# Performance work log

Measured on AMD Instinct MI355X. Metric: run time of the kernel, lower is better.

Reference implementation:

```python
import jax, jax.numpy as jnp
import numpy as np

B, S, H, D = 256, 512, 256, 512  # batch, n_seq, n_hid, n_dim
LN_EPS = 1e-5


def _xavier(key, fan_out, fan_in):
    lim = (6.0 / (fan_in + fan_out)) ** 0.5
    return jax.random.uniform(key, (fan_out, fan_in), jnp.float32, -lim, lim)


def setup_inputs() -> dict:
    key = jax.random.key(0)
    ks = jax.random.split(key, 10)
    x = jax.random.normal(ks[0], (B, S, D), jnp.float32)
    k_w = _xavier(ks[1], H, D)
    q_w = _xavier(ks[2], H, D)
    v_w = _xavier(ks[3], H, D)
    lb = 1.0 / (D ** 0.5)
    k_b = jax.random.uniform(ks[4], (H,), jnp.float32, -lb, lb)
    q_b = jax.random.uniform(ks[5], (H,), jnp.float32, -lb, lb)
    v_b = jax.random.uniform(ks[6], (H,), jnp.float32, -lb, lb)
    attn_bias = jax.random.normal(ks[7], (S, H), jnp.float32)
    ln_g = jnp.ones((H,), jnp.float32)
    ln_b = jnp.zeros((H,), jnp.float32)
    lo = 1.0 / ((S * H) ** 0.5)
    out_w = jax.random.uniform(ks[8], (D, S * H), jnp.float32, -lo, lo)
    out_b = jax.random.uniform(ks[9], (D,), jnp.float32, -lo, lo)
    return {"x": x, "k_w": k_w, "k_b": k_b, "q_w": q_w, "q_b": q_b,
            "v_w": v_w, "v_b": v_b, "attn_bias": attn_bias,
            "ln_g": ln_g, "ln_b": ln_b, "out_w": out_w, "out_b": out_b}


def reference(x, k_w, k_b, q_w, q_b, v_w, v_b, attn_bias, ln_g, ln_b, out_w, out_b):
    # projections: [B,S,D] -> [B,S,H]
    k = jnp.einsum('bsd,hd->bsh', x, k_w) + k_b
    q = jnp.einsum('bsd,hd->bsh', x, q_w) + q_b
    v = jnp.einsum('bsd,hd->bsh', x, v_w) + v_b
    # scores = k^T q, scaled by BATCH size^-0.5 (faithful to v.shape[0]**-0.5)
    scale = x.shape[0] ** (-0.5)
    scores = jnp.einsum('bsh,bsg->bhg', k, q) * scale  # [B,H,H]
    weight = jax.nn.softmax(scores, axis=1)
    out = jnp.einsum('bsh,bhg->bsg', v, weight)  # [B,S,H]
    out = out + attn_bias
    # LayerNorm over last dim
    mu = out.mean(-1, keepdims=True)
    var = out.var(-1, keepdims=True)
    out = (out - mu) * jax.lax.rsqrt(var + LN_EPS) * ln_g + ln_b
    # dropout is identity in eval mode; exact (erf) GELU matches torch default
    out = jax.nn.gelu(out, approximate=False)
    out = out.reshape(out.shape[0], S * H)
    out = out @ out_w.T + out_b  # [B,D]
    return out[:, None, :]  # [B,1,D]
```

## Files before the change

### kernel.cpp

```cpp
#include <hip/hip_runtime.h>
#include <hip/hip_bf16.h>
#include <math.h>

#define B_ 256
#define S_ 512
#define H_ 256
#define D_ 512

typedef __bf16 bf16;
typedef __bf16 bf16x8 __attribute__((ext_vector_type(8)));
typedef float  f32x4  __attribute__((ext_vector_type(4)));
typedef unsigned short u16x8 __attribute__((ext_vector_type(8)));
typedef unsigned short u16x4 __attribute__((ext_vector_type(4)));

#define MFMA(a, b, c) __builtin_amdgcn_mfma_f32_16x16x32_bf16((a), (b), (c), 0, 0, 0)

__device__ __forceinline__ int swz(int row, int kbyte) {
  return (row * 128 + kbyte) ^ ((row & 7) << 4);
}
__device__ __forceinline__ unsigned short bfbits(float f) {
  bf16 h = (bf16)f;
  union { bf16 b; unsigned short u; } c; c.b = h; return c.u;
}
__device__ __forceinline__ bf16x8 cvt8(const float* __restrict__ p) {
  f32x4 a = *(const f32x4*)p;
  f32x4 b = *(const f32x4*)(p + 4);
  bf16x8 r;
  r[0] = (bf16)a[0]; r[1] = (bf16)a[1]; r[2] = (bf16)a[2]; r[3] = (bf16)a[3];
  r[4] = (bf16)b[0]; r[5] = (bf16)b[1]; r[6] = (bf16)b[2]; r[7] = (bf16)b[3];
  return r;
}
__device__ __forceinline__ void gload16(const unsigned short* g, unsigned char* l) {
  __builtin_amdgcn_global_load_lds(
      (const __attribute__((address_space(1))) unsigned int*)g,
      (__attribute__((address_space(3))) unsigned int*)l, 16, 0, 0);
}

__global__ __launch_bounds__(256) void k_convw(
    const float* __restrict__ kw, const float* __restrict__ qw,
    const float* __restrict__ vw, unsigned short* __restrict__ wc)
{
  const int r = blockIdx.x;
  const float* src = (r < 256) ? kw + (size_t)r * 512
                   : (r < 512) ? qw + (size_t)(r - 256) * 512
                               : vw + (size_t)(r - 512) * 512;
  const int c = threadIdx.x * 2;
  wc[(size_t)r * 512 + c]     = bfbits(src[c]);
  wc[(size_t)r * 512 + c + 1] = bfbits(src[c + 1]);
}

__global__ __launch_bounds__(256) void k_proj3(
    const float* __restrict__ x,
    const unsigned short* __restrict__ wc,
    const float* __restrict__ kbi, const float* __restrict__ qbi,
    const float* __restrict__ vbi,
    unsigned short* __restrict__ k_t, unsigned short* __restrict__ q_t,
    unsigned short* __restrict__ v_o, int nwg)
{
  __shared__ __align__(16) unsigned char sA[16384];
  __shared__ __align__(16) unsigned char sB[32768];

  const int o = blockIdx.x;
  const int cpx = nwg >> 3;
  const int a = (o & 7) * cpx + (o >> 3);
  const int mt = a / 6;
  const int nb = a - mt * 6;
  const int m0 = mt * 128;
  const int n0 = nb * 128;
  const int region = nb >> 1;
  const int h0 = (nb & 1) * 128;
  const float* __restrict__ Bi = (region == 0) ? kbi : (region == 1) ? qbi : vbi;

  const int tid = threadIdx.x;
  const int lane = tid & 63;
  const int wid = tid >> 6;
  const int wm = wid >> 1;
  const int wn = wid & 1;
  const int l15 = lane & 15;
  const int lr = lane >> 3;
  const int lk = (lane & 7) << 3;

  f32x4 acc[4][4];
#pragma unroll
  for (int i = 0; i < 4; ++i)
#pragma unroll
    for (int j = 0; j < 4; ++j) acc[i][j] = (f32x4){0.f, 0.f, 0.f, 0.f};

  auto issueB = [&](int kt, int buf) {
#pragma unroll
    for (int i = 0; i < 4; ++i) {
      const int chunk = wid * 4 + i;
      const int row = chunk * 8 + lr;
      gload16(wc + (size_t)(n0 + row) * 512 + kt * 64 + lk,
              sB + buf * 16384 + chunk * 1024);
    }
  };

  f32x4 pa[4], pb[4];
  auto loadA = [&](int kt) {
#pragma unroll
    for (int i = 0; i < 4; ++i) {
      int c = tid + i * 256;
      int row = c >> 3, kc = (c & 7) * 8;
      const float* p = x + (size_t)(m0 + row) * D_ + kt * 64 + kc;
      pa[i] = *(const f32x4*)p;
      pb[i] = *(const f32x4*)(p + 4);
    }
  };

  loadA(0);
  issueB(0, 0);

  for (int kt = 0; kt < 8; ++kt) {
    const int cur = kt & 1;
    __builtin_amdgcn_s_barrier();
    __builtin_amdgcn_sched_barrier(0);
#pragma unroll
    for (int i = 0; i < 4; ++i) {
      int c = tid + i * 256;
      int row = c >> 3, kc = (c & 7) * 8;
      bf16x8 r;
      r[0] = (bf16)pa[i][0]; r[1] = (bf16)pa[i][1];
      r[2] = (bf16)pa[i][2]; r[3] = (bf16)pa[i][3];
      r[4] = (bf16)pb[i][0]; r[5] = (bf16)pb[i][1];
      r[6] = (bf16)pb[i][2]; r[7] = (bf16)pb[i][3];
      *(bf16x8*)(sA + swz(row, kc * 2)) = r;
    }
    if (kt < 7) issueB(kt + 1, cur ^ 1);
    if (kt < 7) asm volatile("s_waitcnt vmcnt(4) lgkmcnt(0)" ::: "memory");
    else        asm volatile("s_waitcnt vmcnt(0) lgkmcnt(0)" ::: "memory");
    __builtin_amdgcn_s_barrier();
    __builtin_amdgcn_sched_barrier(0);
    if (kt < 7) loadA(kt + 1);
#pragma unroll
    for (int ks = 0; ks < 2; ++ks) {
      const int kb2 = ks * 64 + ((lane >> 4) << 4);
      bf16x8 av[4], bv[4];
#pragma unroll
      for (int f = 0; f < 4; ++f)
        av[f] = *(const bf16x8*)(sA + swz(wm * 64 + f * 16 + l15, kb2));
#pragma unroll
      for (int f = 0; f < 4; ++f)
        bv[f] = *(const bf16x8*)(sB + cur * 16384 + (wn * 64 + f * 16 + l15) * 128 + kb2);
#pragma unroll
      for (int fm = 0; fm < 4; ++fm)
#pragma unroll
        for (int fn = 0; fn < 4; ++fn)
          acc[fm][fn] = MFMA(av[fm], bv[fn], acc[fm][fn]);
    }
    __builtin_amdgcn_sched_barrier(0);
  }

  const int b = m0 >> 9;
  const int sbase = m0 & 511;
  const int r4 = (lane >> 4) * 4;
#pragma unroll
  for (int fn = 0; fn < 4; ++fn) {
    const int hcol = h0 + wn * 64 + fn * 16 + l15;
    const float bias = Bi[hcol];
#pragma unroll
    for (int fm = 0; fm < 4; ++fm) {
      const int s = sbase + wm * 64 + fm * 16 + r4;
      if (region < 2) {
        unsigned short* dst = ((region == 0) ? k_t : q_t) +
                              (size_t)b * (H_ * S_) + (size_t)hcol * S_ + s;
        u16x4 ov;
#pragma unroll
        for (int j = 0; j < 4; ++j) ov[j] = bfbits(acc[fm][fn][j] + bias);
        *(u16x4*)dst = ov;
      } else {
#pragma unroll
        for (int j = 0; j < 4; ++j)
          v_o[(size_t)b * (S_ * H_) + (size_t)(s + j) * H_ + hcol] =
              bfbits(acc[fm][fn][j] + bias);
      }
    }
  }
}

__global__ __launch_bounds__(1024, 4) void k_attn(
    const unsigned short* __restrict__ k_t,
    const unsigned short* __restrict__ q_t,
    const unsigned short* __restrict__ v_o,
    const float* __restrict__ attn_bias,
    const float* __restrict__ lng, const float* __restrict__ lnb,
    unsigned short* __restrict__ act)
{
  __shared__ __align__(16) unsigned char sm[163840];
  unsigned char* sP = sm;
  float* redm = (float*)(sm + 131072);
  float* reds = (float*)(sm + 131072 + 4096);
  float* lbuf = (float*)(sm + 147456);

  const int tid = threadIdx.x;
  const int lane = tid & 63;
  const int wid = tid >> 6;
  const int l15 = lane & 15;
  const int l16 = lane >> 4;
  const int b = blockIdx.x;
  const int wh = wid >> 2;
  const int wq = wid & 3;

  const unsigned short* __restrict__ Kb = k_t + (size_t)b * (H_ * S_);
  const unsigned short* __restrict__ Qb = q_t + (size_t)b * (H_ * S_);
  const unsigned short* __restrict__ Vb = v_o + (size_t)b * (S_ * H_);

  const int srow8 = lane >> 3;
  const int scol16 = (lane & 7) ^ srow8;

  auto stage1 = [&](int t, int buf) {
#pragma unroll
    for (int i = 0; i < 2; ++i) {
      const int cb = wid * 2 + i;
      const int row = cb * 8 + srow8;
      gload16(Kb + (size_t)row * S_ + t * 64 + scol16 * 8,
              sm + buf * 65536 + cb * 1024);
      gload16(Qb + (size_t)row * S_ + t * 64 + scol16 * 8,
              sm + buf * 65536 + 32768 + cb * 1024);
    }
  };

  f32x4 acc1[4][4];
#pragma unroll
  for (int i = 0; i < 4; ++i)
#pragma unroll
    for (int j = 0; j < 4; ++j) acc1[i][j] = (f32x4){0.f, 0.f, 0.f, 0.f};

  stage1(0, 0);
  for (int t = 0; t < 8; ++t) {
    const int cur = t & 1;
    if (t < 7) stage1(t + 1, cur ^ 1);
    if (t < 7) asm volatile("s_waitcnt vmcnt(4)" ::: "memory");
    else       asm volatile("s_waitcnt vmcnt(0)" ::: "memory");
    __builtin_amdgcn_s_barrier();
    __builtin_amdgcn_sched_barrier(0);
    const unsigned char* sK = sm + cur * 65536;
    const unsigned char* sQ = sK + 32768;
#pragma unroll
    for (int ks = 0; ks < 2; ++ks) {
      const int kb2 = ks * 64 + l16 * 16;
      bf16x8 av[4], bv[4];
#pragma unroll
      for (int f = 0; f < 4; ++f)
        av[f] = *(const bf16x8*)(sK + swz(wh * 64 + f * 16 + l15, kb2));
#pragma unroll
      for (int f = 0; f < 4; ++f)
        bv[f] = *(const bf16x8*)(sQ + swz(wq * 64 + f * 16 + l15, kb2));
#pragma unroll
      for (int fm = 0; fm < 4; ++fm)
#pragma unroll
        for (int fn = 0; fn < 4; ++fn)
          acc1[fm][fn] = MFMA(av[fm], bv[fn], acc1[fm][fn]);
    }
    __builtin_amdgcn_sched_barrier(0);
    __builtin_amdgcn_s_barrier();
  }

  float cmax[4] = {-3.0e38f, -3.0e38f, -3.0e38f, -3.0e38f};
#pragma unroll
  for (int fm = 0; fm < 4; ++fm)
#pragma unroll
    for (int fn = 0; fn < 4; ++fn)
#pragma unroll
      for (int j = 0; j < 4; ++j) {
        acc1[fm][fn][j] *= 0.0625f;
        cmax[fn] = fmaxf(cmax[fn], acc1[fm][fn][j]);
      }
#pragma unroll
  for (int fn = 0; fn < 4; ++fn) {
    cmax[fn] = fmaxf(cmax[fn], __shfl_xor(cmax[fn], 16));
    cmax[fn] = fmaxf(cmax[fn], __shfl_xor(cmax[fn], 32));
  }
  if (lane < 16) {
#pragma unroll
    for (int fn = 0; fn < 4; ++fn)
      redm[wh * 256 + wq * 64 + fn * 16 + lane] = cmax[fn];
  }
  __syncthreads();
  float gmax[4];
#pragma unroll
  for (int fn = 0; fn < 4; ++fn) {
    const int c = wq * 64 + fn * 16 + l15;
    gmax[fn] = fmaxf(fmaxf(redm[c], redm[256 + c]),
                     fmaxf(redm[512 + c], redm[768 + c]));
  }
  float csum[4] = {0.f, 0.f, 0.f, 0.f};
#pragma unroll
  for (int fm = 0; fm < 4; ++fm)
#pragma unroll
    for (int fn = 0; fn < 4; ++fn)
#pragma unroll
      for (int j = 0; j < 4; ++j) {
        float p = __expf(acc1[fm][fn][j] - gmax[fn]);
        acc1[fm][fn][j] = p;
        csum[fn] += p;
      }
#pragma unroll
  for (int fn = 0; fn < 4; ++fn) {
    csum[fn] += __shfl_xor(csum[fn], 16);
    csum[fn] += __shfl_xor(csum[fn], 32);
  }
  if (lane < 16) {
#pragma unroll
    for (int fn = 0; fn < 4; ++fn)
      reds[wh * 256 + wq * 64 + fn * 16 + lane] = csum[fn];
  }
  __syncthreads();
  float gi[4];
#pragma unroll
  for (int fn = 0; fn < 4; ++fn) {
    const int c = wq * 64 + fn * 16 + l15;
    gi[fn] = 1.0f / (reds[c] + reds[256 + c] + reds[512 + c] + reds[768 + c]);
  }

#pragma unroll
  for (int fn = 0; fn < 4; ++fn) {
    const int g = wq * 64 + fn * 16 + l15;
#pragma unroll
    for (int fm = 0; fm < 4; ++fm) {
      const int h0 = wh * 64 + fm * 16 + l16 * 4;
      u16x4 pv;
#pragma unroll
      for (int j = 0; j < 4; ++j) pv[j] = bfbits(acc1[fm][fn][j] * gi[fn]);
      *(u16x4*)(sP + ((g * 512 + h0 * 2) ^ ((g & 7) << 4))) = pv;
    }
  }
  __syncthreads();

  const int vrow = tid >> 2;
  const int vcol16 = (tid & 3) ^ ((vrow >> 1) & 3);

  auto stageV = [&](int t) {
    const int so_ = t >> 3, kh_ = t & 7;
    gload16(Vb + (size_t)(so_ * 256 + vrow) * H_ + kh_ * 32 + vcol16 * 8,
            sm + 131072 + (t & 1) * 16384 + wid * 1024);
  };

  f32x4 acc2[4][4];
  stageV(0);
  for (int t = 0; t < 16; ++t) {
    const int so = t >> 3, kh = t & 7, cur = t & 1;
    if (kh == 0) {
#pragma unroll
      for (int i = 0; i < 4; ++i)
#pragma unroll
        for (int j = 0; j < 4; ++j) acc2[i][j] = (f32x4){0.f, 0.f, 0.f, 0.f};
    }
    if (t < 15) stageV(t + 1);
    if (t < 15) asm volatile("s_waitcnt vmcnt(1)" ::: "memory");
    else        asm volatile("s_waitcnt vmcnt(0)" ::: "memory");
    __builtin_amdgcn_s_barrier();
    __builtin_amdgcn_sched_barrier(0);
    const unsigned char* sV = sm + 131072 + cur * 16384;
    bf16x8 av[4], bv[4];
#pragma unroll
    for (int f = 0; f < 4; ++f) {
      const int rl = wh * 64 + f * 16 + l15;
      av[f] = *(const bf16x8*)(sV + rl * 64 + ((l16 ^ ((rl >> 1) & 3)) << 4));
    }
#pragma unroll
    for (int fn = 0; fn < 4; ++fn) {
      const int g = wq * 64 + fn * 16 + l15;
      bv[fn] = *(const bf16x8*)(
          sP + ((g * 512 + kh * 64 + l16 * 16) ^ ((g & 7) << 4)));
    }
#pragma unroll
    for (int f = 0; f < 4; ++f)
#pragma unroll
      for (int fn = 0; fn < 4; ++fn)
        acc2[f][fn] = MFMA(av[f], bv[fn], acc2[f][fn]);
    __builtin_amdgcn_sched_barrier(0);

    if (kh == 7) {
      __syncthreads();
#pragma unroll
      for (int f = 0; f < 4; ++f) {
#pragma unroll
        for (int j = 0; j < 4; ++j) {
          const int rloc = wh * 64 + f * 16 + l16 * 4 + j;
          const int s = so * 256 + rloc;
          float ps = 0.f, psq = 0.f;
#pragma unroll
          for (int fn = 0; fn < 4; ++fn) {
            const int g = wq * 64 + fn * 16 + l15;
            float vv = acc2[f][fn][j] + attn_bias[(size_t)s * H_ + g];
            acc2[f][fn][j] = vv;
            ps += vv; psq += vv * vv;
          }
          ps += __shfl_xor(ps, 1);  psq += __shfl_xor(psq, 1);
          ps += __shfl_xor(ps, 2);  psq += __shfl_xor(psq, 2);
          ps += __shfl_xor(ps, 4);  psq += __shfl_xor(psq, 4);
          ps += __shfl_xor(ps, 8);  psq += __shfl_xor(psq, 8);
          if (l15 == 0) {
            lbuf[wq * 256 + rloc] = ps;
            lbuf[1024 + wq * 256 + rloc] = psq;
          }
        }
      }
      __syncthreads();
#pragma unroll
      for (int f = 0; f < 4; ++f) {
#pragma unroll
        for (int j = 0; j < 4; ++j) {
          const int rloc = wh * 64 + f * 16 + l16 * 4 + j;
          const int s = so * 256 + rloc;
          float sum = lbuf[rloc] + lbuf[256 + rloc] +
                      lbuf[512 + rloc] + lbuf[768 + rloc];
          float sq  = lbuf[1024 + rloc] + lbuf[1280 + rloc] +
                      lbuf[1536 + rloc] + lbuf[1792 + rloc];
          float mu = sum * (1.f / H_);
          float var = sq * (1.f / H_) - mu * mu;
          float rstd = rsqrtf(var + 1e-5f);
#pragma unroll
          for (int fn = 0; fn < 4; ++fn) {
            const int g = wq * 64 + fn * 16 + l15;
            float xv = (acc2[f][fn][j] - mu) * rstd * lng[g] + lnb[g];
            float y = 0.5f * xv * (1.f + erff(xv * 0.70710678118654752f));
            act[(size_t)b * (S_ * H_) + (size_t)s * H_ + g] = bfbits(y);
          }
        }
      }
      __syncthreads();
    } else {
      __builtin_amdgcn_s_barrier();
    }
  }
}

__global__ __launch_bounds__(512) void k_final(
    const unsigned short* __restrict__ act,
    const float* __restrict__ ow,
    float* __restrict__ partial)
{
  __shared__ __align__(16) unsigned char sA[256 * 128];
  __shared__ __align__(16) unsigned char sB[64 * 128];

  const int tid = threadIdx.x;
  const int lane = tid & 63;
  const int wid = tid >> 6;
  const int wm = wid >> 1;
  const int wn = wid & 1;
  const int n0 = blockIdx.x * 64;
  const size_t k0 = (size_t)blockIdx.y * 4096;

  f32x4 acc[4][2];
#pragma unroll
  for (int i = 0; i < 4; ++i)
#pragma unroll
    for (int j = 0; j < 2; ++j) acc[i][j] = (f32x4){0.f, 0.f, 0.f, 0.f};

  for (int kt = 0; kt < 64; ++kt) {
    const size_t kb = k0 + kt * 64;
    __syncthreads();
#pragma unroll
    for (int i = 0; i < 4; ++i) {
      int c = tid + i * 512;
      int row = c >> 3, kc = (c & 7) * 8;
      *(u16x8*)(sA + swz(row, kc * 2)) =
          *(const u16x8*)(act + (size_t)row * 131072 + kb + kc);
    }
    {
      int row = tid >> 3, kc = (tid & 7) * 8;
      *(bf16x8*)(sB + swz(row, kc * 2)) =
          cvt8(ow + (size_t)(n0 + row) * 131072 + kb + kc);
    }
    __syncthreads();
#pragma unroll
    for (int ks = 0; ks < 2; ++ks) {
      const int kbyte = ks * 64 + (lane >> 4) * 16;
      bf16x8 av[4], bv[2];
#pragma unroll
      for (int f = 0; f < 4; ++f)
        av[f] = *(const bf16x8*)(sA + swz(wm * 64 + f * 16 + (lane & 15), kbyte));
#pragma unroll
      for (int f = 0; f < 2; ++f)
        bv[f] = *(const bf16x8*)(sB + swz(wn * 32 + f * 16 + (lane & 15), kbyte));
#pragma unroll
      for (int fm = 0; fm < 4; ++fm)
#pragma unroll
        for (int fn = 0; fn < 2; ++fn)
          acc[fm][fn] = MFMA(av[fm], bv[fn], acc[fm][fn]);
    }
  }

  float* __restrict__ P = partial + (size_t)blockIdx.y * (256 * 512);
  const int r4 = (lane >> 4) * 4;
#pragma unroll
  for (int fn = 0; fn < 2; ++fn) {
    int col = n0 + wn * 32 + fn * 16 + (lane & 15);
#pragma unroll
    for (int fm = 0; fm < 4; ++fm) {
      int mb = wm * 64 + fm * 16 + r4;
#pragma unroll
      for (int j = 0; j < 4; ++j)
        P[(size_t)(mb + j) * 512 + col] = acc[fm][fn][j];
    }
  }
}

__global__ __launch_bounds__(256) void k_reduce(
    const float* __restrict__ partial,
    const float* __restrict__ ob,
    float* __restrict__ out)
{
  const int i4 = blockIdx.x * 256 + threadIdx.x;
  f32x4 s = *(const f32x4*)(ob + ((i4 & 127) << 2));
#pragma unroll
  for (int ks = 0; ks < 32; ++ks)
    s += *(const f32x4*)(partial + (size_t)ks * 131072 + (size_t)i4 * 4);
  *(f32x4*)(out + (size_t)i4 * 4) = s;
}

extern "C" void kernel_launch(void* const* d_in, const int* in_sizes, int n_in,
                              void* d_out, int out_size, void* d_ws, size_t ws_size,
                              hipStream_t stream) {
  const float* x         = (const float*)d_in[0];
  const float* k_w       = (const float*)d_in[1];
  const float* k_b       = (const float*)d_in[2];
  const float* q_w       = (const float*)d_in[3];
  const float* q_b       = (const float*)d_in[4];
  const float* v_w       = (const float*)d_in[5];
  const float* v_b       = (const float*)d_in[6];
  const float* attn_bias = (const float*)d_in[7];
  const float* ln_g      = (const float*)d_in[8];
  const float* ln_b      = (const float*)d_in[9];
  const float* out_w     = (const float*)d_in[10];
  const float* out_b     = (const float*)d_in[11];
  float* out = (float*)d_out;

  char* ws = (char*)d_ws;
  unsigned short* k_t = (unsigned short*)(ws);
  unsigned short* q_t = (unsigned short*)(ws + 67108864);
  unsigned short* v_o = (unsigned short*)(ws + 134217728);
  unsigned short* wc  = (unsigned short*)(ws + 201326592);
  unsigned short* act = k_t;
  float* partial      = (float*)(ws + 67108864);

  k_convw<<<dim3(768), dim3(256), 0, stream>>>(k_w, q_w, v_w, wc);

  const int nwg = 6144;
  k_proj3<<<dim3(nwg), dim3(256), 0, stream>>>(
      x, wc, k_b, q_b, v_b, k_t, q_t, v_o, nwg);

  k_attn<<<dim3(256), dim3(1024), 0, stream>>>(
      k_t, q_t, v_o, attn_bias, ln_g, ln_b, act);

  k_final<<<dim3(8, 32), dim3(512), 0, stream>>>(act, out_w, partial);
  k_reduce<<<dim3(128), dim3(256), 0, stream>>>(partial, out_b, out);
}
```

Baseline: 519.4 us.

## Pre-swizzle converted weights and single-buffer B tile in projection GEMM

The weight conversion kernel now writes bf16 weights already XOR-swizzled per row, so the projection kernel can read its B tile from LDS with the same swizzled addressing as A and avoid bank conflicts. The projection kernel drops double buffering of the B tile (halving its LDS) and replaces the manual waitcnt/barrier pipeline with plain __syncthreads after a synchronous load. This trades prefetch overlap of B for lower LDS use, possibly higher occupancy, and conflict-free B fragment reads.

```diff
diff --git a/kernel.cpp b/kernel.cpp
--- a/kernel.cpp
+++ b/kernel.cpp
@@ -44,12 +44,15 @@
   const float* src = (r < 256) ? kw + (size_t)r * 512
                    : (r < 512) ? qw + (size_t)(r - 256) * 512
                                : vw + (size_t)(r - 512) * 512;
-  const int c = threadIdx.x * 2;
-  wc[(size_t)r * 512 + c]     = bfbits(src[c]);
-  wc[(size_t)r * 512 + c + 1] = bfbits(src[c + 1]);
-}
-
-__global__ __launch_bounds__(256) void k_proj3(
+#pragma unroll
+  for (int q = 0; q < 2; ++q) {
+    const int c = threadIdx.x * 2 + q;
+    const int sc = (c & ~63) | (((((c >> 3) & 7) ^ (r & 7))) << 3) | (c & 7);
+    wc[(size_t)r * 512 + c] = bfbits(src[sc]);
+  }
+}
+
+__global__ __launch_bounds__(256) void k_proj2(
     const float* __restrict__ x,
     const unsigned short* __restrict__ wc,
     const float* __restrict__ kbi, const float* __restrict__ qbi,
@@ -58,7 +61,7 @@
     unsigned short* __restrict__ v_o, int nwg)
 {
   __shared__ __align__(16) unsigned char sA[16384];
-  __shared__ __align__(16) unsigned char sB[32768];
+  __shared__ __align__(16) unsigned char sB[16384];
 
   const int o = blockIdx.x;
   const int cpx = nwg >> 3;
@@ -86,16 +89,6 @@
 #pragma unroll
     for (int j = 0; j < 4; ++j) acc[i][j] = (f32x4){0.f, 0.f, 0.f, 0.f};
 
-  auto issueB = [&](int kt, int buf) {
-#pragma unroll
-    for (int i = 0; i < 4; ++i) {
-      const int chunk = wid * 4 + i;
-      const int row = chunk * 8 + lr;
-      gload16(wc + (size_t)(n0 + row) * 512 + kt * 64 + lk,
-              sB + buf * 16384 + chunk * 1024);
-    }
-  };
-
   f32x4 pa[4], pb[4];
   auto loadA = [&](int kt) {
 #pragma unroll
@@ -109,12 +102,9 @@
   };
 
   loadA(0);
-  issueB(0, 0);
 
   for (int kt = 0; kt < 8; ++kt) {
-    const int cur = kt & 1;
-    __builtin_amdgcn_s_barrier();
-    __builtin_amdgcn_sched_barrier(0);
+    if (kt) __syncthreads();
 #pragma unroll
     for (int i = 0; i < 4; ++i) {
       int c = tid + i * 256;
@@ -126,11 +116,13 @@
       r[6] = (bf16)pb[i][2]; r[7] = (bf16)pb[i][3];
       *(bf16x8*)(sA + swz(row, kc * 2)) = r;
     }
-    if (kt < 7) issueB(kt + 1, cur ^ 1);
-    if (kt < 7) asm volatile("s_waitcnt vmcnt(4) lgkmcnt(0)" ::: "memory");
-    else        asm volatile("s_waitcnt vmcnt(0) lgkmcnt(0)" ::: "memory");
-    __builtin_amdgcn_s_barrier();
-    __builtin_amdgcn_sched_barrier(0);
+#pragma unroll
+    for (int i = 0; i < 4; ++i) {
+      const int chunk = wid * 4 + i;
+      const int row = chunk * 8 + lr;
+      gload16(wc + (size_t)(n0 + row) * 512 + kt * 64 + lk, sB + chunk * 1024);
+    }
+    __syncthreads();
     if (kt < 7) loadA(kt + 1);
 #pragma unroll
     for (int ks = 0; ks < 2; ++ks) {
@@ -141,14 +133,13 @@
         av[f] = *(const bf16x8*)(sA + swz(wm * 64 + f * 16 + l15, kb2));
 #pragma unroll
       for (int f = 0; f < 4; ++f)
-        bv[f] = *(const bf16x8*)(sB + cur * 16384 + (wn * 64 + f * 16 + l15) * 128 + kb2);
+        bv[f] = *(const bf16x8*)(sB + swz(wn * 64 + f * 16 + l15, kb2));
 #pragma unroll
       for (int fm = 0; fm < 4; ++fm)
 #pragma unroll
         for (int fn = 0; fn < 4; ++fn)
           acc[fm][fn] = MFMA(av[fm], bv[fn], acc[fm][fn]);
     }
-    __builtin_amdgcn_sched_barrier(0);
   }
 
   const int b = m0 >> 9;
@@ -539,7 +530,7 @@
   k_convw<<<dim3(768), dim3(256), 0, stream>>>(k_w, q_w, v_w, wc);
 
   const int nwg = 6144;
-  k_proj3<<<dim3(nwg), dim3(256), 0, stream>>>(
+  k_proj2<<<dim3(nwg), dim3(256), 0, stream>>>(
       x, wc, k_b, q_b, v_b, k_t, q_t, v_o, nwg);
 
   k_attn<<<dim3(256), dim3(1024), 0, stream>>>(
```

Result: faster. 495.7 us (-4.6%).
